# Kernel tuning notes

Measured on AMD Instinct MI355X. Metric: run time of the kernel, lower is better.

Reference implementation:

```python
import jax, jax.numpy as jnp
import numpy as np

# neuralef_loss_cfg constants (kernel = '10nnn_sigm1.0')
T = 10.0        # cfg['t']
ALPHA = 0.05    # cfg['alpha']
KNN = 10        # parsed from '10nnn'
SIGMA2 = 1.0    # parsed from 'sigm1.0'
EPS = 1e-12     # F.normalize eps

N_TOKENS, D_FEAT, K_EIG = 8192, 768, 256


def setup_inputs() -> dict:
    key = jax.random.key(0)
    k1, k2 = jax.random.split(key)
    FF = jax.random.normal(k1, (N_TOKENS, D_FEAT), dtype=jnp.float32)
    Psi = jax.random.normal(k2, (N_TOKENS, K_EIG), dtype=jnp.float32)
    return {"FF": FF, "Psi": Psi}


def _gram_knn(FF):
    """torch.no_grad() block: RBF affinity -> topk KNN sparsify -> sym -> degree norm."""
    # input_l2_normalize: F.normalize(FF, dim=1)
    FFn = FF / jnp.maximum(jnp.linalg.norm(FF, axis=1, keepdims=True), EPS)
    sq = jnp.sum(FFn * FFn, axis=-1)                       # [N]
    # pairwise squared distances -> RBF kernel  [N, N]
    A = jnp.exp(-(sq[:, None] + sq[None, :] - 2.0 * (FFn @ FFn.T)) / (2.0 * SIGMA2))
    vals, idx = jax.lax.top_k(A, KNN)                      # [N, KNN]
    N = A.shape[0]
    rows = jnp.arange(N)
    # res.scatter_(1, idx, vals) on zeros_like(A)
    res = jnp.zeros_like(A).at[rows[:, None], idx].set(vals)
    gram = 0.5 * (res + res.T)
    gram = gram.at[rows, rows].set(0.0)                    # zero diagonal
    Dsum = jnp.sum(gram, axis=-1)
    # D = Dsum.rsqrt(); D[D==inf] = 0  (Dsum >= 0 always since vals >= 0)
    D = jnp.where(Dsum > 0, jax.lax.rsqrt(Dsum), 0.0)
    return D[:, None] * gram * D[None, :]


def reference(FF, Psi):
    N = Psi.shape[0]
    Psi = Psi * (T / N)
    gram = jax.lax.stop_gradient(_gram_knn(FF))            # [N, N]
    gPsi = gram @ Psi                                      # [N, K]
    R = Psi.T @ gPsi                                       # [K, K]
    # no_sg = False: R_hat = Psi.T.detach() @ gram @ Psi
    R_hat = jax.lax.stop_gradient(Psi).T @ gPsi
    loss = -jnp.trace(R)
    reg = jnp.sum(jnp.triu(R_hat ** 2, 1))
    return jnp.stack([loss, reg * ALPHA])
```

## Files before the change

### kernel.cpp

```cpp
#include <hip/hip_runtime.h>
#include <math.h>

#define N_TOK 8192
#define D_FEAT 768
#define K_EIG 256
#define KNN 10
#define CAP 256
#define NCHUNK 4
#define CHUNK 2048

typedef unsigned short ushort_t;
typedef float f32x4 __attribute__((ext_vector_type(4)));
typedef short bf16x8 __attribute__((ext_vector_type(8)));
typedef unsigned short u16x8 __attribute__((ext_vector_type(8)));
typedef unsigned short u16x4 __attribute__((ext_vector_type(4)));

__device__ inline float u2f(unsigned u) { union { unsigned u; float f; } c; c.u = u; return c.f; }
__device__ inline unsigned f2u(float f) { union { unsigned u; float f; } c; c.f = f; return c.u; }
__device__ inline ushort_t f2bf_rne(float f) {
  const unsigned u = f2u(f);
  return (ushort_t)((u + 0x7fffu + ((u >> 16) & 1u)) >> 16);
}
__device__ inline ushort_t f2key(float f) {
  const unsigned h = f2u(f) >> 16;
  return (ushort_t)((h & 0x8000u) ? (h ^ 0xFFFFu) : (h | 0x8000u));
}
__device__ inline float key2f(unsigned k) {
  const unsigned h = (k & 0x8000u) ? (k ^ 0x8000u) : (k ^ 0xFFFFu);
  return u2f(h << 16);
}
__device__ inline unsigned wave_max_u32(unsigned m) {
#pragma unroll
  for (int s = 1; s < 64; s <<= 1) m = max(m, (unsigned)__shfl_xor((int)m, s, 64));
  return m;
}

__global__ __launch_bounds__(192) void k_norm(const float* __restrict__ FF,
                                              ushort_t* __restrict__ FFbf,
                                              float* __restrict__ rn,
                                              float* __restrict__ sqv) {
  const int row = blockIdx.x;
  const int tid = threadIdx.x;
  const float4 v = *(const float4*)&FF[(size_t)row * D_FEAT + tid * 4];
  float s = v.x * v.x + v.y * v.y + v.z * v.z + v.w * v.w;
  __shared__ float red[3];
  for (int m = 32; m > 0; m >>= 1) s += __shfl_xor(s, m, 64);
  if ((tid & 63) == 0) red[tid >> 6] = s;
  __syncthreads();
  const float tot = red[0] + red[1] + red[2];
  const float scale = 1.f / fmaxf(sqrtf(tot), 1e-12f);
  float4 w;
  w.x = v.x * scale; w.y = v.y * scale; w.z = v.z * scale; w.w = v.w * scale;
  float s2 = w.x * w.x + w.y * w.y + w.z * w.z + w.w * w.w;
  u16x4 o;
  o[0] = f2bf_rne(w.x); o[1] = f2bf_rne(w.y); o[2] = f2bf_rne(w.z); o[3] = f2bf_rne(w.w);
  *(u16x4*)&FFbf[(size_t)row * D_FEAT + tid * 4] = o;
  for (int m = 32; m > 0; m >>= 1) s2 += __shfl_xor(s2, m, 64);
  __syncthreads();
  if ((tid & 63) == 0) red[tid >> 6] = s2;
  __syncthreads();
  if (tid == 0) { sqv[row] = red[0] + red[1] + red[2]; rn[row] = scale; }
}

#define AS1(p) ((const __attribute__((address_space(1))) void*)(p))
#define AS3(p) ((__attribute__((address_space(3))) void*)(p))

__global__ __launch_bounds__(512) void k_gemm(const ushort_t* __restrict__ FFbf,
                                              ushort_t* __restrict__ Cs,
                                              ushort_t* __restrict__ Gmax,
                                              int cbase) {
  __shared__ ushort_t smem[32768];
  const int tid = threadIdx.x;
  const int swz = ((int)blockIdx.x & 7) * 64 + ((int)blockIdx.x >> 3);
  const int mb = swz >> 4;
  const int nb = swz & 15;
  const int rbase = mb * 256;
  const int cb = cbase + nb * 128;
  const int w = tid >> 6, lane = tid & 63;
  const int wr = w >> 1, wc = w & 1;
  const int fr = lane & 15, kg = lane >> 4;
  const int srow = tid >> 2, skq = tid & 3;

  f32x4 acc[4][4];
#pragma unroll
  for (int m = 0; m < 4; ++m)
#pragma unroll
    for (int n = 0; n < 4; ++n) acc[m][n] = (f32x4){0.f, 0.f, 0.f, 0.f};

#define STAGE(b, kt) do { \
    const ushort_t* ga = FFbf + (size_t)(rbase + srow) * D_FEAT + (kt) * 32 + skq * 8; \
    const ushort_t* gb = FFbf + (size_t)(cb + srow) * D_FEAT + (kt) * 32 + skq * 8; \
    char* ab = (char*)smem + (b) * 16384; \
    char* bb = (char*)smem + 32768 + (b) * 8192; \
    __builtin_amdgcn_global_load_lds(AS1(ga), AS3(ab + tid * 16), 16, 0, 0); \
    __builtin_amdgcn_global_load_lds(AS1(ga + (size_t)128 * D_FEAT), AS3(ab + 8192 + tid * 16), 16, 0, 0); \
    __builtin_amdgcn_global_load_lds(AS1(gb), AS3(bb + tid * 16), 16, 0, 0); \
  } while (0)

  STAGE(0, 0);
  int buf = 0;
  for (int kt = 0; kt < D_FEAT / 32; ++kt) {
    __syncthreads();
    if (kt + 1 < D_FEAT / 32) STAGE(buf ^ 1, kt + 1);
    bf16x8 af[4], bfr[4];
#pragma unroll
    for (int m = 0; m < 4; ++m)
      af[m] = *(const bf16x8*)&smem[buf * 8192 + (wr * 64 + m * 16 + fr) * 32 + kg * 8];
#pragma unroll
    for (int n = 0; n < 4; ++n)
      bfr[n] = *(const bf16x8*)&smem[16384 + buf * 4096 + (wc * 64 + n * 16 + fr) * 32 + kg * 8];
#pragma unroll
    for (int m = 0; m < 4; ++m)
#pragma unroll
      for (int n = 0; n < 4; ++n)
        acc[m][n] = __builtin_amdgcn_mfma_f32_16x16x32_bf16(af[m], bfr[n], acc[m][n], 0, 0, 0);
    buf ^= 1;
  }
#undef STAGE

  __syncthreads();
#pragma unroll
  for (int m = 0; m < 4; ++m)
#pragma unroll
    for (int n = 0; n < 4; ++n)
#pragma unroll
      for (int r = 0; r < 4; ++r)
        smem[(wr * 64 + m * 16 + kg * 4 + r) * 128 + wc * 64 + n * 16 + fr] = f2key(acc[m][n][r]);
  __syncthreads();
#pragma unroll
  for (int i = 0; i < 8; ++i) {
    const int off = i * 8192 + tid * 16;
    const int row = off >> 8;
    const int colb = off & 255;
    const u16x8 v = *(const u16x8*)((const char*)smem + off);
    *(u16x8*)((char*)Cs + (size_t)(rbase + row) * (CHUNK * 2) + (size_t)nb * 256 + colb) = v;
  }
  {
    const int r2 = tid >> 1;
    const int half = tid & 1;
    u16x8 gmv;
#pragma unroll
    for (int g = 0; g < 8; ++g) {
      const u16x8 grp = *(const u16x8*)&smem[r2 * 128 + half * 64 + g * 8];
      unsigned mx = 0;
#pragma unroll
      for (int j = 0; j < 8; ++j) mx = max(mx, (unsigned)(ushort_t)grp[j]);
      gmv[g] = (ushort_t)mx;
    }
    *(u16x8*)&Gmax[(size_t)(rbase + r2) * 256 + nb * 16 + half * 8] = gmv;
  }
}

__global__ __launch_bounds__(256) void k_sel(const ushort_t* __restrict__ Cs,
                                             const ushort_t* __restrict__ Gmax,
                                             int chunk,
                                             float* __restrict__ pd, int* __restrict__ pi) {
  const int tid = threadIdx.x;
  const int lane = tid & 63;
  const int row = blockIdx.x * 4 + (tid >> 6);
  const ushort_t* src = Cs + (size_t)row * CHUNK;

  const u16x4 gm = *(const u16x4*)&Gmax[(size_t)row * 256 + lane * 4];
  unsigned cur[4];
#pragma unroll
  for (int k = 0; k < 4; ++k)
    cur[k] = (((unsigned)(ushort_t)gm[k]) << 16) | (unsigned)(lane * 4 + k);
  unsigned keep = 0;
#pragma unroll
  for (int r = 0; r < 16; ++r) {
    unsigned m = max(max(cur[0], cur[1]), max(cur[2], cur[3]));
    m = wave_max_u32(m);
    if (lane == r) keep = m;
    const unsigned gid = m & 0xFFu;
    if (lane == (int)(gid >> 2)) {
      const int sl = (int)(gid & 3u);
#pragma unroll
      for (int k = 0; k < 4; ++k)
        if (k == sl) cur[k] = 0;
    }
  }
  const unsigned gid2 = keep & 0xFFu;
  unsigned E[8];
  if (lane < 16) {
    const u16x8 g = *(const u16x8*)&src[gid2 * 8];
#pragma unroll
    for (int j = 0; j < 8; ++j)
      E[j] = (((unsigned)(ushort_t)g[j]) << 16) | (gid2 * 8 + (unsigned)j);
  } else {
#pragma unroll
    for (int j = 0; j < 8; ++j) E[j] = 0;
  }
  unsigned keep2 = 0;
#pragma unroll
  for (int r = 0; r < 16; ++r) {
    unsigned m = E[0];
#pragma unroll
    for (int j = 1; j < 8; ++j) m = max(m, E[j]);
    m = wave_max_u32(m);
    if (lane == r) keep2 = m;
    const unsigned col = m & 0xFFFFu;
    const bool mine = (lane < 16) && ((col >> 3) == gid2);
    const int sl = (int)(col & 7u);
#pragma unroll
    for (int j = 0; j < 8; ++j)
      if (mine && j == sl) E[j] = 0;
  }
  if (lane < 16) {
    pd[((size_t)row * NCHUNK + chunk) * 16 + lane] = key2f(keep2 >> 16);
    pi[((size_t)row * NCHUNK + chunk) * 16 + lane] = chunk * CHUNK + (int)(keep2 & 0xFFFFu);
  }
}

__global__ __launch_bounds__(256) void k_rescore(const float* __restrict__ FF,
                                                 const float* __restrict__ rn,
                                                 const float* __restrict__ sqv,
                                                 const float* __restrict__ pd,
                                                 const int* __restrict__ pi,
                                                 float* __restrict__ tv, int* __restrict__ tj) {
  const int tid = threadIdx.x;
  const int lane = tid & 63;
  const int row = blockIdx.x * 4 + (tid >> 6);

  const float pdv = pd[(size_t)row * 64 + lane];
  const int myj = pi[(size_t)row * 64 + lane];
  unsigned cur = (((unsigned)f2key(pdv)) << 16) | (unsigned)lane;
  int selj = 0;
#pragma unroll
  for (int r = 0; r < 16; ++r) {
    const unsigned m = wave_max_u32(cur);
    const int wln = (int)(m & 63u);
    const int jw = __shfl(myj, wln, 64);
    if (lane == r) selj = jw;
    if (lane == wln) cur = 0;
  }

  const float si = rn[row];
  const float sqi = sqv[row];
  const float* fi = FF + (size_t)row * D_FEAT;
  float4 a0 = *(const float4*)&fi[lane * 4];
  float4 a1 = *(const float4*)&fi[256 + lane * 4];
  float4 a2 = *(const float4*)&fi[512 + lane * 4];
  a0.x *= si; a0.y *= si; a0.z *= si; a0.w *= si;
  a1.x *= si; a1.y *= si; a1.z *= si; a1.w *= si;
  a2.x *= si; a2.y *= si; a2.z *= si; a2.w *= si;

  float dsc_l = 0.f, dvl_l = 0.f; int j_l = 0;
#pragma unroll 4
  for (int c = 0; c < 16; ++c) {
    const int j = __shfl(selj, c, 64);
    const float sj = rn[j];
    const float* fj = FF + (size_t)j * D_FEAT;
    const float4 b0 = *(const float4*)&fj[lane * 4];
    const float4 b1 = *(const float4*)&fj[256 + lane * 4];
    const float4 b2 = *(const float4*)&fj[512 + lane * 4];
    float acc = 0.f;
    acc = fmaf(a0.x, b0.x * sj, acc); acc = fmaf(a0.y, b0.y * sj, acc);
    acc = fmaf(a0.z, b0.z * sj, acc); acc = fmaf(a0.w, b0.w * sj, acc);
    acc = fmaf(a1.x, b1.x * sj, acc); acc = fmaf(a1.y, b1.y * sj, acc);
    acc = fmaf(a1.z, b1.z * sj, acc); acc = fmaf(a1.w, b1.w * sj, acc);
    acc = fmaf(a2.x, b2.x * sj, acc); acc = fmaf(a2.y, b2.y * sj, acc);
    acc = fmaf(a2.z, b2.z * sj, acc); acc = fmaf(a2.w, b2.w * sj, acc);
#pragma unroll
    for (int m = 32; m > 0; m >>= 1) acc += __shfl_xor(acc, m, 64);
    if (lane == c) {
      const float sqj = sqv[j];
      j_l = j;
      dsc_l = acc - 0.5f * sqj;
      dvl_l = expf(-0.5f * (sqi + sqj - 2.f * acc));
    }
  }

  unsigned fk = 0;
  if (lane < 16) {
    const unsigned u = f2u(dsc_l);
    fk = u ^ ((u >> 31) ? 0xFFFFFFFFu : 0x80000000u);
  }
#pragma unroll
  for (int s = 0; s < 10; ++s) {
    const unsigned m = wave_max_u32(fk);
    const unsigned long long bal = __ballot(fk == m);
    const int wln = __ffsll((unsigned long long)bal) - 1;
    const float tvv = __shfl(dvl_l, wln, 64);
    const int tjj = __shfl(j_l, wln, 64);
    if (lane == s) {
      tv[(size_t)row * KNN + s] = tvv;
      tj[(size_t)row * KNN + s] = tjj;
    }
    if (lane == wln) fk = 0;
  }
}

__global__ void k_scatter(const float* __restrict__ tv, const int* __restrict__ tj,
                          int* __restrict__ cnt, int* __restrict__ nbrJ,
                          float* __restrict__ nbrW) {
  const int e = blockIdx.x * blockDim.x + threadIdx.x;
  if (e >= N_TOK * KNN) return;
  const int i = e / KNN;
  const int j = tj[e];
  if (j == i) return;
  const float w = 0.5f * tv[e];
  const int p = atomicAdd(&cnt[i], 1);
  if (p < CAP) { nbrJ[(size_t)i * CAP + p] = j; nbrW[(size_t)i * CAP + p] = w; }
  const int q = atomicAdd(&cnt[j], 1);
  if (q < CAP) { nbrJ[(size_t)j * CAP + q] = i; nbrW[(size_t)j * CAP + q] = w; }
}

__global__ void k_degree(const int* __restrict__ cnt, const float* __restrict__ nbrW,
                         float* __restrict__ Dv) {
  const int r = blockIdx.x * 4 + (threadIdx.x >> 6);
  const int lane = threadIdx.x & 63;
  const int c = min(cnt[r], CAP);
  float s = 0.f;
  for (int m = lane; m < c; m += 64) s += nbrW[(size_t)r * CAP + m];
  for (int m = 32; m > 0; m >>= 1) s += __shfl_xor(s, m, 64);
  if (lane == 0) Dv[r] = (s > 0.f) ? rsqrtf(s) : 0.f;
}

__global__ __launch_bounds__(256) void k_gpsi(const float* __restrict__ Psi,
                                              const int* __restrict__ cnt,
                                              const int* __restrict__ nbrJ,
                                              const float* __restrict__ nbrW,
                                              const float* __restrict__ Dv,
                                              float* __restrict__ gP) {
  const int i = blockIdx.x;
  const int tid = threadIdx.x;
  __shared__ int sJ[CAP];
  __shared__ float sW[CAP];
  const int c = min(cnt[i], CAP);
  if (tid < c) {
    const int j = nbrJ[(size_t)i * CAP + tid];
    sJ[tid] = j;
    sW[tid] = nbrW[(size_t)i * CAP + tid] * Dv[j];
  }
  __syncthreads();
  float acc = 0.f;
  for (int m = 0; m < c; ++m) acc += sW[m] * Psi[(size_t)sJ[m] * K_EIG + tid];
  gP[(size_t)i * K_EIG + tid] = acc * Dv[i];
}

__global__ __launch_bounds__(256) void k_Rpart(const float* __restrict__ Psi,
                                               const float* __restrict__ gP,
                                               float* __restrict__ Rp) {
  __shared__ float sP[64][68];
  __shared__ float sG[64][68];
  const int tid = threadIdx.x;
  const int ks = blockIdx.x >> 4;
  const int tile = blockIdx.x & 15;
  const int at = (tile >> 2) * 64;
  const int bt = (tile & 3) * 64;
  const int a4 = (tid & 15) * 4;
  const int b4 = (tid >> 4) * 4;
  const int lr = tid >> 2;

  float acc[4][4];
#pragma unroll
  for (int i = 0; i < 4; ++i)
#pragma unroll
    for (int j = 0; j < 4; ++j) acc[i][j] = 0.f;

  for (int rt = 0; rt < 8; ++rt) {
    const int r0 = ks * 512 + rt * 64;
    __syncthreads();
#pragma unroll
    for (int q = 0; q < 4; ++q) {
      const int seg = (tid & 3) + q * 4;
      *(float4*)&sP[lr][seg * 4] = *(const float4*)&Psi[(size_t)(r0 + lr) * K_EIG + at + seg * 4];
      *(float4*)&sG[lr][seg * 4] = *(const float4*)&gP[(size_t)(r0 + lr) * K_EIG + bt + seg * 4];
    }
    __syncthreads();
#pragma unroll 4
    for (int r = 0; r < 64; ++r) {
      const float4 pa = *(const float4*)&sP[r][a4];
      const float4 pg = *(const float4*)&sG[r][b4];
      acc[0][0] = fmaf(pa.x, pg.x, acc[0][0]); acc[0][1] = fmaf(pa.x, pg.y, acc[0][1]);
      acc[0][2] = fmaf(pa.x, pg.z, acc[0][2]); acc[0][3] = fmaf(pa.x, pg.w, acc[0][3]);
      acc[1][0] = fmaf(pa.y, pg.x, acc[1][0]); acc[1][1] = fmaf(pa.y, pg.y, acc[1][1]);
      acc[1][2] = fmaf(pa.y, pg.z, acc[1][2]); acc[1][3] = fmaf(pa.y, pg.w, acc[1][3]);
      acc[2][0] = fmaf(pa.z, pg.x, acc[2][0]); acc[2][1] = fmaf(pa.z, pg.y, acc[2][1]);
      acc[2][2] = fmaf(pa.z, pg.z, acc[2][2]); acc[2][3] = fmaf(pa.z, pg.w, acc[2][3]);
      acc[3][0] = fmaf(pa.w, pg.x, acc[3][0]); acc[3][1] = fmaf(pa.w, pg.y, acc[3][1]);
      acc[3][2] = fmaf(pa.w, pg.z, acc[3][2]); acc[3][3] = fmaf(pa.w, pg.w, acc[3][3]);
    }
  }
#pragma unroll
  for (int i = 0; i < 4; ++i) {
    float4 o; o.x = acc[i][0]; o.y = acc[i][1]; o.z = acc[i][2]; o.w = acc[i][3];
    *(float4*)&Rp[(size_t)ks * (K_EIG * K_EIG) + (size_t)(at + a4 + i) * K_EIG + bt + b4] = o;
  }
}

__global__ __launch_bounds__(256) void k_Rred(const float* __restrict__ Rp,
                                              double* __restrict__ part) {
  const int tid = threadIdx.x;
  const int e0 = blockIdx.x * 1024 + tid * 4;
  float4 s = {0.f, 0.f, 0.f, 0.f};
  for (int ks = 0; ks < 16; ++ks) {
    const float4 v = *(const float4*)&Rp[(size_t)ks * (K_EIG * K_EIG) + e0];
    s.x += v.x; s.y += v.y; s.z += v.z; s.w += v.w;
  }
  const float sc = (10.f / 8192.f) * (10.f / 8192.f);
  double tl = 0.0, rg = 0.0;
#pragma unroll
  for (int j = 0; j < 4; ++j) {
    const int e = e0 + j;
    const int a = e >> 8, b = e & 255;
    const double v = (double)(((const float*)&s)[j] * sc);
    if (a == b) tl += v;
    else if (b > a) rg += v * v;
  }
  __shared__ double st[256], sr[256];
  st[tid] = tl; sr[tid] = rg;
  __syncthreads();
  for (int w = 128; w > 0; w >>= 1) {
    if (tid < w) { st[tid] += st[tid + w]; sr[tid] += sr[tid + w]; }
    __syncthreads();
  }
  if (tid == 0) { part[blockIdx.x] = st[0]; part[64 + blockIdx.x] = sr[0]; }
}

__global__ void k_final2(const double* __restrict__ part, float* __restrict__ out) {
  const int lane = threadIdx.x;
  double tl = part[lane];
  double rg = part[64 + lane];
  for (int m = 32; m > 0; m >>= 1) {
    tl += __shfl_xor(tl, m, 64);
    rg += __shfl_xor(rg, m, 64);
  }
  if (lane == 0) {
    out[0] = (float)(-tl);
    out[1] = (float)(rg * 0.05);
  }
}

extern "C" void kernel_launch(void* const* d_in, const int* in_sizes, int n_in,
                              void* d_out, int out_size, void* d_ws, size_t ws_size,
                              hipStream_t stream) {
  const float* FF = (const float*)d_in[0];
  const float* Psi = (const float*)d_in[1];
  float* out = (float*)d_out;
  float* ws = (float*)d_ws;

  size_t o = 0;
  ushort_t* FFbf = (ushort_t*)(ws + o); o += (size_t)N_TOK * D_FEAT / 2;
  float* rn  = ws + o; o += N_TOK;
  float* sqv = ws + o; o += N_TOK;
  float* pd  = ws + o; o += (size_t)N_TOK * NCHUNK * 16;
  int*   pi  = (int*)(ws + o); o += (size_t)N_TOK * NCHUNK * 16;
  float* tv  = ws + o; o += (size_t)N_TOK * KNN;
  int*   tj  = (int*)(ws + o); o += (size_t)N_TOK * KNN;
  int*   cnt = (int*)(ws + o); o += N_TOK;
  double* part = (double*)(ws + o); o += 256;
  ushort_t* Gmax = (ushort_t*)(ws + o); o += (size_t)N_TOK * 256 / 2;
  char* X = (char*)(ws + o);
  ushort_t* Cs = (ushort_t*)X;
  int*   nbrJ = (int*)X;
  float* nbrW = (float*)(X + (size_t)N_TOK * CAP * 4);
  float* Dv   = (float*)(X + 2 * (size_t)N_TOK * CAP * 4);
  float* gP   = (float*)(X + 2 * (size_t)N_TOK * CAP * 4 + (size_t)N_TOK * 4);
  float* Rp   = (float*)(X + 25ull * 1024 * 1024);

  k_norm<<<N_TOK, 192, 0, stream>>>(FF, FFbf, rn, sqv);
  for (int c = 0; c < NCHUNK; ++c) {
    k_gemm<<<(N_TOK / 256) * (CHUNK / 128), 512, 0, stream>>>(FFbf, Cs, Gmax, c * CHUNK);
    k_sel<<<N_TOK / 4, 256, 0, stream>>>(Cs, Gmax, c, pd, pi);
  }
  k_rescore<<<N_TOK / 4, 256, 0, stream>>>(FF, rn, sqv, pd, pi, tv, tj);
  hipMemsetAsync(cnt, 0, N_TOK * sizeof(int), stream);
  k_scatter<<<(N_TOK * KNN + 255) / 256, 256, 0, stream>>>(tv, tj, cnt, nbrJ, nbrW);
  k_degree<<<N_TOK / 4, 256, 0, stream>>>(cnt, nbrW, Dv);
  k_gpsi<<<N_TOK, 256, 0, stream>>>(Psi, cnt, nbrJ, nbrW, Dv, gP);
  k_Rpart<<<256, 256, 0, stream>>>(Psi, gP, Rp);
  k_Rred<<<64, 256, 0, stream>>>(Rp, part);
  k_final2<<<1, 64, 0, stream>>>(part, out);
}
```

Baseline: 365.3 us.

## Triple-buffer GEMM K-loop with vmcnt waits and fold cnt memset into rescore

The bf16 GEMM mainloop moves from double to triple buffering in LDS. It uses explicit s_waitcnt vmcnt(3) plus a raw barrier so the next tile's global-to-LDS loads stay in flight during the MFMA work, and raises wave priority around the MFMA block. The hipMemsetAsync of the neighbor counters is dropped and done inside k_rescore instead, removing one launch, and the rescore loop unroll goes from 4 to 8. The extra LDS buffer (72KB per block) may lower occupancy, and the hand-written waitcnt logic relies on the compiler not reordering other memory ops.

```diff
diff --git a/kernel.cpp b/kernel.cpp
--- a/kernel.cpp
+++ b/kernel.cpp
@@ -69,7 +69,7 @@
                                               ushort_t* __restrict__ Cs,
                                               ushort_t* __restrict__ Gmax,
                                               int cbase) {
-  __shared__ ushort_t smem[32768];
+  __shared__ ushort_t smem[36864];
   const int tid = threadIdx.x;
   const int swz = ((int)blockIdx.x & 7) * 64 + ((int)blockIdx.x >> 3);
   const int mb = swz >> 4;
@@ -91,31 +91,49 @@
     const ushort_t* ga = FFbf + (size_t)(rbase + srow) * D_FEAT + (kt) * 32 + skq * 8; \
     const ushort_t* gb = FFbf + (size_t)(cb + srow) * D_FEAT + (kt) * 32 + skq * 8; \
     char* ab = (char*)smem + (b) * 16384; \
-    char* bb = (char*)smem + 32768 + (b) * 8192; \
+    char* bb = (char*)smem + 49152 + (b) * 8192; \
     __builtin_amdgcn_global_load_lds(AS1(ga), AS3(ab + tid * 16), 16, 0, 0); \
     __builtin_amdgcn_global_load_lds(AS1(ga + (size_t)128 * D_FEAT), AS3(ab + 8192 + tid * 16), 16, 0, 0); \
     __builtin_amdgcn_global_load_lds(AS1(gb), AS3(bb + tid * 16), 16, 0, 0); \
   } while (0)
 
+#define COMPUTE(b) do { \
+    bf16x8 af[4], bfr[4]; \
+    _Pragma("unroll") \
+    for (int m = 0; m < 4; ++m) \
+      af[m] = *(const bf16x8*)&smem[(b) * 8192 + (wr * 64 + m * 16 + fr) * 32 + kg * 8]; \
+    _Pragma("unroll") \
+    for (int n = 0; n < 4; ++n) \
+      bfr[n] = *(const bf16x8*)&smem[24576 + (b) * 4096 + (wc * 64 + n * 16 + fr) * 32 + kg * 8]; \
+    __builtin_amdgcn_s_setprio(1); \
+    _Pragma("unroll") \
+    for (int m = 0; m < 4; ++m) \
+      _Pragma("unroll") \
+      for (int n = 0; n < 4; ++n) \
+        acc[m][n] = __builtin_amdgcn_mfma_f32_16x16x32_bf16(af[m], bfr[n], acc[m][n], 0, 0, 0); \
+    __builtin_amdgcn_s_setprio(0); \
+  } while (0)
+
+#define KSTEP(bR, bS, kt) do { \
+    if ((kt) + 1 < 24) { \
+      STAGE(bS, (kt) + 1); \
+      asm volatile("s_waitcnt vmcnt(3)" ::: "memory"); \
+    } else { \
+      asm volatile("s_waitcnt vmcnt(0)" ::: "memory"); \
+    } \
+    __builtin_amdgcn_s_barrier(); \
+    __builtin_amdgcn_sched_barrier(0); \
+    COMPUTE(bR); \
+  } while (0)
+
   STAGE(0, 0);
-  int buf = 0;
-  for (int kt = 0; kt < D_FEAT / 32; ++kt) {
-    __syncthreads();
-    if (kt + 1 < D_FEAT / 32) STAGE(buf ^ 1, kt + 1);
-    bf16x8 af[4], bfr[4];
-#pragma unroll
-    for (int m = 0; m < 4; ++m)
-      af[m] = *(const bf16x8*)&smem[buf * 8192 + (wr * 64 + m * 16 + fr) * 32 + kg * 8];
-#pragma unroll
-    for (int n = 0; n < 4; ++n)
-      bfr[n] = *(const bf16x8*)&smem[16384 + buf * 4096 + (wc * 64 + n * 16 + fr) * 32 + kg * 8];
-#pragma unroll
-    for (int m = 0; m < 4; ++m)
-#pragma unroll
-      for (int n = 0; n < 4; ++n)
-        acc[m][n] = __builtin_amdgcn_mfma_f32_16x16x32_bf16(af[m], bfr[n], acc[m][n], 0, 0, 0);
-    buf ^= 1;
-  }
+  for (int kb = 0; kb < 24; kb += 3) {
+    KSTEP(0, 1, kb);
+    KSTEP(1, 2, kb + 1);
+    KSTEP(2, 0, kb + 2);
+  }
+#undef KSTEP
+#undef COMPUTE
 #undef STAGE
 
   __syncthreads();
@@ -216,10 +234,12 @@
                                                  const float* __restrict__ sqv,
                                                  const float* __restrict__ pd,
                                                  const int* __restrict__ pi,
-                                                 float* __restrict__ tv, int* __restrict__ tj) {
+                                                 float* __restrict__ tv, int* __restrict__ tj,
+                                                 int* __restrict__ cnt) {
   const int tid = threadIdx.x;
   const int lane = tid & 63;
   const int row = blockIdx.x * 4 + (tid >> 6);
+  if (lane == 0) cnt[row] = 0;
 
   const float pdv = pd[(size_t)row * 64 + lane];
   const int myj = pi[(size_t)row * 64 + lane];
@@ -245,7 +265,7 @@
   a2.x *= si; a2.y *= si; a2.z *= si; a2.w *= si;
 
   float dsc_l = 0.f, dvl_l = 0.f; int j_l = 0;
-#pragma unroll 4
+#pragma unroll 8
   for (int c = 0; c < 16; ++c) {
     const int j = __shfl(selj, c, 64);
     const float sj = rn[j];
@@ -464,8 +484,7 @@
     k_gemm<<<(N_TOK / 256) * (CHUNK / 128), 512, 0, stream>>>(FFbf, Cs, Gmax, c * CHUNK);
     k_sel<<<N_TOK / 4, 256, 0, stream>>>(Cs, Gmax, c, pd, pi);
   }
-  k_rescore<<<N_TOK / 4, 256, 0, stream>>>(FF, rn, sqv, pd, pi, tv, tj);
-  hipMemsetAsync(cnt, 0, N_TOK * sizeof(int), stream);
+  k_rescore<<<N_TOK / 4, 256, 0, stream>>>(FF, rn, sqv, pd, pi, tv, tj, cnt);
   k_scatter<<<(N_TOK * KNN + 255) / 256, 256, 0, stream>>>(tv, tj, cnt, nbrJ, nbrW);
   k_degree<<<N_TOK / 4, 256, 0, stream>>>(cnt, nbrW, Dv);
   k_gpsi<<<N_TOK, 256, 0, stream>>>(Psi, cnt, nbrJ, nbrW, Dv, gP);
```

Result: faster. 351.4 us, median of 2 (-3.8%).

## Enlarge GEMM tile to 256x256 with XOR-swizzled LDS and fused cnt reset

Applied to the files above, without the earlier changes.

Rebuilds the similarity GEMM around a 256x256 output tile with a K-step of 64, a 128 KB double-buffered LDS held in an XOR-swizzled layout, explicit vmcnt waits and raw barriers, and raised wave priority around the MFMA block. The aim is more arithmetic intensity per LDS load, fewer bank conflicts and better overlap of global-to-LDS copies with compute. It also moves the cnt zeroing into k_rescore so the separate memset is gone, and unrolls the rescore loop further. The larger LDS and accumulator footprint lowers occupancy and adds register pressure.

```diff
diff --git a/kernel.cpp b/kernel.cpp
--- a/kernel.cpp
+++ b/kernel.cpp
@@ -69,85 +69,115 @@
                                               ushort_t* __restrict__ Cs,
                                               ushort_t* __restrict__ Gmax,
                                               int cbase) {
-  __shared__ ushort_t smem[32768];
-  const int tid = threadIdx.x;
-  const int swz = ((int)blockIdx.x & 7) * 64 + ((int)blockIdx.x >> 3);
-  const int mb = swz >> 4;
-  const int nb = swz & 15;
+  __shared__ ushort_t smem[65536];
+  const int tid = threadIdx.x;
+  const int swz = ((int)blockIdx.x & 7) * 32 + ((int)blockIdx.x >> 3);
+  const int mb = swz >> 3;
+  const int nb = swz & 7;
   const int rbase = mb * 256;
-  const int cb = cbase + nb * 128;
+  const int cb = cbase + nb * 256;
   const int w = tid >> 6, lane = tid & 63;
-  const int wr = w >> 1, wc = w & 1;
+  const int wr = w >> 2;
+  const int wc = w & 3;
   const int fr = lane & 15, kg = lane >> 4;
-  const int srow = tid >> 2, skq = tid & 3;
-
-  f32x4 acc[4][4];
-#pragma unroll
-  for (int m = 0; m < 4; ++m)
+  const int h8 = fr & 7;
+  const int slot0 = ((kg ^ h8) * 16);
+  const int slot1 = slot0 ^ 64;
+  const int srow = tid >> 3;
+  const int scol = (((tid & 7) ^ ((tid >> 3) & 7)) * 8);
+
+  f32x4 acc[8][4];
+#pragma unroll
+  for (int m = 0; m < 8; ++m)
 #pragma unroll
     for (int n = 0; n < 4; ++n) acc[m][n] = (f32x4){0.f, 0.f, 0.f, 0.f};
 
 #define STAGE(b, kt) do { \
-    const ushort_t* ga = FFbf + (size_t)(rbase + srow) * D_FEAT + (kt) * 32 + skq * 8; \
-    const ushort_t* gb = FFbf + (size_t)(cb + srow) * D_FEAT + (kt) * 32 + skq * 8; \
-    char* ab = (char*)smem + (b) * 16384; \
-    char* bb = (char*)smem + 32768 + (b) * 8192; \
+    const ushort_t* ga = FFbf + (size_t)(rbase + srow) * D_FEAT + (kt) * 64 + scol; \
+    const ushort_t* gb = FFbf + (size_t)(cb + srow) * D_FEAT + (kt) * 64 + scol; \
+    char* ab = (char*)smem + (b) * 32768; \
+    char* bb = (char*)smem + 65536 + (b) * 32768; \
     __builtin_amdgcn_global_load_lds(AS1(ga), AS3(ab + tid * 16), 16, 0, 0); \
-    __builtin_amdgcn_global_load_lds(AS1(ga + (size_t)128 * D_FEAT), AS3(ab + 8192 + tid * 16), 16, 0, 0); \
+    __builtin_amdgcn_global_load_lds(AS1(ga + (size_t)64 * D_FEAT), AS3(ab + 8192 + tid * 16), 16, 0, 0); \
+    __builtin_amdgcn_global_load_lds(AS1(ga + (size_t)128 * D_FEAT), AS3(ab + 16384 + tid * 16), 16, 0, 0); \
+    __builtin_amdgcn_global_load_lds(AS1(ga + (size_t)192 * D_FEAT), AS3(ab + 24576 + tid * 16), 16, 0, 0); \
     __builtin_amdgcn_global_load_lds(AS1(gb), AS3(bb + tid * 16), 16, 0, 0); \
+    __builtin_amdgcn_global_load_lds(AS1(gb + (size_t)64 * D_FEAT), AS3(bb + 8192 + tid * 16), 16, 0, 0); \
+    __builtin_amdgcn_global_load_lds(AS1(gb + (size_t)128 * D_FEAT), AS3(bb + 16384 + tid * 16), 16, 0, 0); \
+    __builtin_amdgcn_global_load_lds(AS1(gb + (size_t)192 * D_FEAT), AS3(bb + 24576 + tid * 16), 16, 0, 0); \
   } while (0)
 
   STAGE(0, 0);
-  int buf = 0;
-  for (int kt = 0; kt < D_FEAT / 32; ++kt) {
-    __syncthreads();
-    if (kt + 1 < D_FEAT / 32) STAGE(buf ^ 1, kt + 1);
-    bf16x8 af[4], bfr[4];
-#pragma unroll
-    for (int m = 0; m < 4; ++m)
-      af[m] = *(const bf16x8*)&smem[buf * 8192 + (wr * 64 + m * 16 + fr) * 32 + kg * 8];
+  for (int t = 0; t < 12; ++t) {
+    const int cur = t & 1;
+    if (t + 1 < 12) {
+      STAGE(cur ^ 1, t + 1);
+      asm volatile("s_waitcnt vmcnt(8)" ::: "memory");
+    } else {
+      asm volatile("s_waitcnt vmcnt(0)" ::: "memory");
+    }
+    __builtin_amdgcn_s_barrier();
+    __builtin_amdgcn_sched_barrier(0);
+    {
+      const char* abuf = (const char*)smem + cur * 32768;
+      const char* bbuf = (const char*)smem + 65536 + cur * 32768;
+      bf16x8 bfr[4][2];
+#pragma unroll
+      for (int n = 0; n < 4; ++n) {
+        const int brow = (wc * 64 + n * 16 + fr) * 128;
+        bfr[n][0] = *(const bf16x8*)(bbuf + brow + slot0);
+        bfr[n][1] = *(const bf16x8*)(bbuf + brow + slot1);
+      }
+      __builtin_amdgcn_s_setprio(1);
+#pragma unroll
+      for (int m = 0; m < 8; ++m) {
+        const int arow = (wr * 128 + m * 16 + fr) * 128;
+        const bf16x8 af0 = *(const bf16x8*)(abuf + arow + slot0);
+        const bf16x8 af1 = *(const bf16x8*)(abuf + arow + slot1);
+#pragma unroll
+        for (int n = 0; n < 4; ++n) {
+          acc[m][n] = __builtin_amdgcn_mfma_f32_16x16x32_bf16(af0, bfr[n][0], acc[m][n], 0, 0, 0);
+          acc[m][n] = __builtin_amdgcn_mfma_f32_16x16x32_bf16(af1, bfr[n][1], acc[m][n], 0, 0, 0);
+        }
+      }
+      __builtin_amdgcn_s_setprio(0);
+    }
+    __builtin_amdgcn_s_barrier();
+  }
+#undef STAGE
+
+#pragma unroll
+  for (int m = 0; m < 8; ++m)
 #pragma unroll
     for (int n = 0; n < 4; ++n)
-      bfr[n] = *(const bf16x8*)&smem[16384 + buf * 4096 + (wc * 64 + n * 16 + fr) * 32 + kg * 8];
-#pragma unroll
-    for (int m = 0; m < 4; ++m)
-#pragma unroll
-      for (int n = 0; n < 4; ++n)
-        acc[m][n] = __builtin_amdgcn_mfma_f32_16x16x32_bf16(af[m], bfr[n], acc[m][n], 0, 0, 0);
-    buf ^= 1;
-  }
-#undef STAGE
-
+#pragma unroll
+      for (int r = 0; r < 4; ++r)
+        smem[(wr * 128 + m * 16 + kg * 4 + r) * 256 + wc * 64 + n * 16 + fr] = f2key(acc[m][n][r]);
   __syncthreads();
 #pragma unroll
-  for (int m = 0; m < 4; ++m)
-#pragma unroll
-    for (int n = 0; n < 4; ++n)
-#pragma unroll
-      for (int r = 0; r < 4; ++r)
-        smem[(wr * 64 + m * 16 + kg * 4 + r) * 128 + wc * 64 + n * 16 + fr] = f2key(acc[m][n][r]);
-  __syncthreads();
-#pragma unroll
-  for (int i = 0; i < 8; ++i) {
+  for (int i = 0; i < 16; ++i) {
     const int off = i * 8192 + tid * 16;
-    const int row = off >> 8;
-    const int colb = off & 255;
+    const int row = off >> 9;
+    const int colb = off & 511;
     const u16x8 v = *(const u16x8*)((const char*)smem + off);
-    *(u16x8*)((char*)Cs + (size_t)(rbase + row) * (CHUNK * 2) + (size_t)nb * 256 + colb) = v;
+    *(u16x8*)((char*)Cs + (size_t)(rbase + row) * (CHUNK * 2) + (size_t)nb * 512 + colb) = v;
   }
   {
     const int r2 = tid >> 1;
-    const int half = tid & 1;
-    u16x8 gmv;
-#pragma unroll
-    for (int g = 0; g < 8; ++g) {
-      const u16x8 grp = *(const u16x8*)&smem[r2 * 128 + half * 64 + g * 8];
-      unsigned mx = 0;
-#pragma unroll
-      for (int j = 0; j < 8; ++j) mx = max(mx, (unsigned)(ushort_t)grp[j]);
-      gmv[g] = (ushort_t)mx;
-    }
-    *(u16x8*)&Gmax[(size_t)(rbase + r2) * 256 + nb * 16 + half * 8] = gmv;
+    const int gh = (tid & 1) * 16;
+#pragma unroll
+    for (int gg = 0; gg < 2; ++gg) {
+      u16x8 gmv;
+#pragma unroll
+      for (int g2 = 0; g2 < 8; ++g2) {
+        const u16x8 grp = *(const u16x8*)&smem[r2 * 256 + (gh + gg * 8 + g2) * 8];
+        unsigned mx = 0;
+#pragma unroll
+        for (int j = 0; j < 8; ++j) mx = max(mx, (unsigned)(ushort_t)grp[j]);
+        gmv[g2] = (ushort_t)mx;
+      }
+      *(u16x8*)&Gmax[(size_t)(rbase + r2) * 256 + nb * 32 + gh + gg * 8] = gmv;
+    }
   }
 }
 
@@ -216,10 +246,12 @@
                                                  const float* __restrict__ sqv,
                                                  const float* __restrict__ pd,
                                                  const int* __restrict__ pi,
-                                                 float* __restrict__ tv, int* __restrict__ tj) {
+                                                 float* __restrict__ tv, int* __restrict__ tj,
+                                                 int* __restrict__ cnt) {
   const int tid = threadIdx.x;
   const int lane = tid & 63;
   const int row = blockIdx.x * 4 + (tid >> 6);
+  if (lane == 0) cnt[row] = 0;
 
   const float pdv = pd[(size_t)row * 64 + lane];
   const int myj = pi[(size_t)row * 64 + lane];
@@ -245,7 +277,7 @@
   a2.x *= si; a2.y *= si; a2.z *= si; a2.w *= si;
 
   float dsc_l = 0.f, dvl_l = 0.f; int j_l = 0;
-#pragma unroll 4
+#pragma unroll 8
   for (int c = 0; c < 16; ++c) {
     const int j = __shfl(selj, c, 64);
     const float sj = rn[j];
@@ -461,11 +493,10 @@
 
   k_norm<<<N_TOK, 192, 0, stream>>>(FF, FFbf, rn, sqv);
   for (int c = 0; c < NCHUNK; ++c) {
-    k_gemm<<<(N_TOK / 256) * (CHUNK / 128), 512, 0, stream>>>(FFbf, Cs, Gmax, c * CHUNK);
+    k_gemm<<<(N_TOK / 256) * (CHUNK / 256), 512, 0, stream>>>(FFbf, Cs, Gmax, c * CHUNK);
     k_sel<<<N_TOK / 4, 256, 0, stream>>>(Cs, Gmax, c, pd, pi);
   }
-  k_rescore<<<N_TOK / 4, 256, 0, stream>>>(FF, rn, sqv, pd, pi, tv, tj);
-  hipMemsetAsync(cnt, 0, N_TOK * sizeof(int), stream);
+  k_rescore<<<N_TOK / 4, 256, 0, stream>>>(FF, rn, sqv, pd, pi, tv, tj, cnt);
   k_scatter<<<(N_TOK * KNN + 255) / 256, 256, 0, stream>>>(tv, tj, cnt, nbrJ, nbrW);
   k_degree<<<N_TOK / 4, 256, 0, stream>>>(cnt, nbrW, Dv);
   k_gpsi<<<N_TOK, 256, 0, stream>>>(Psi, cnt, nbrJ, nbrW, Dv, gP);
```

New measurement: 340.2 us (median of 2 runs). 1.07x faster.
